# Kernel tuning notes

Hardware: AMD Instinct MI355X
Metric: run time of the kernel (lower is better)

The kernel has to match this reference:

```python
import jax, jax.numpy as jnp
import numpy as np

WINDOW_SIZE = 11
SIGMA = 1.5
C1 = 0.01 ** 2
C2 = 0.03 ** 2


def _gaussian_1d(window_size, sigma):
    x = np.arange(window_size, dtype=np.float32)
    g = np.exp(-((x - window_size // 2) ** 2) / (2.0 * sigma ** 2))
    g = g / g.sum()
    return jnp.asarray(g, dtype=jnp.float32)


def _blur(x, g1d):
    # Separable depthwise Gaussian blur, SAME padding.
    # x: [B, C, H, W]; mathematically identical to conv with outer(g, g).
    c = x.shape[1]
    pad = WINDOW_SIZE // 2
    kh = jnp.broadcast_to(g1d.reshape(1, 1, WINDOW_SIZE, 1), (c, 1, WINDOW_SIZE, 1))
    kw = jnp.broadcast_to(g1d.reshape(1, 1, 1, WINDOW_SIZE), (c, 1, 1, WINDOW_SIZE))
    dn = ('NCHW', 'OIHW', 'NCHW')
    x = jax.lax.conv_general_dilated(x, kh, (1, 1), [(pad, pad), (0, 0)],
                                     dimension_numbers=dn, feature_group_count=c)
    x = jax.lax.conv_general_dilated(x, kw, (1, 1), [(0, 0), (pad, pad)],
                                     dimension_numbers=dn, feature_group_count=c)
    return x


def setup_inputs() -> dict:
    key = jax.random.key(0)
    k1, k2 = jax.random.split(key)
    shape = (32, 1, 512, 512)
    img1 = jax.random.uniform(k1, shape, dtype=jnp.float32)
    img2 = jax.random.uniform(k2, shape, dtype=jnp.float32)
    return {"img1": img1, "img2": img2}


def reference(img1, img2):
    g1d = _gaussian_1d(WINDOW_SIZE, SIGMA)
    mu1 = _blur(img1, g1d)
    mu2 = _blur(img2, g1d)
    mu1_sq = mu1 * mu1
    mu2_sq = mu2 * mu2
    mu1_mu2 = mu1 * mu2
    sigma1_sq = _blur(img1 * img1, g1d) - mu1_sq
    sigma2_sq = _blur(img2 * img2, g1d) - mu2_sq
    sigma12 = _blur(img1 * img2, g1d) - mu1_mu2
    ssim_map = ((2.0 * mu1_mu2 + C1) * (2.0 * sigma12 + C2)) / (
        (mu1_sq + mu2_sq + C1) * (sigma1_sq + sigma2_sq + C2))
    return ssim_map.mean()  # size_average=True
```

## Files before the change

### kernel.cpp

```cpp
#include <hip/hip_runtime.h>

#define HH 512
#define WW 512
#define BATCH 32
#define BH 16
#define NB (HH / BH)
#define TPB 256
#define NBLOCKS (NB * BATCH)
#define CBASE 0xAAAAAAAAu


__global__ __launch_bounds__(TPB) void ssim_main(
    const float* __restrict__ img1,
    const float* __restrict__ img2,
    unsigned* __restrict__ counter,
    float* __restrict__ partial,
    float* __restrict__ out)
{
  constexpr float G[11] = {
      0.00102838f, 0.00759876f, 0.03600077f, 0.10936070f, 0.21300553f,
      0.26601171f,
      0.21300553f, 0.10936070f, 0.03600077f, 0.00759876f, 0.00102838f};
  constexpr float C1 = 1.0e-4f;
  constexpr float C2 = 9.0e-4f;

  const int tid  = threadIdx.x;
  const int L    = tid & 63;
  const int rr   = tid >> 6;
  const int band = blockIdx.x;
  const int bat  = blockIdx.y;
  const int r0   = band * BH;
  const float* p1 = img1 + (size_t)bat * (HH * WW);
  const float* p2 = img2 + (size_t)bat * (HH * WW);
  const int c0 = tid * 2;

  __shared__ __align__(16) float4 pbuf4[4 * 5 * 128];
  float* sp = (float*)pbuf4;

  const int wu4  = tid >> 1;
  const int wOff = ((wu4 ^ ((wu4 >> 3) & 1)) << 2) + ((tid & 1) << 1);

  const int uLo = (2 * L - 2 < 0) ? 0 : 2 * L - 2;
  const int u0  = (2 * L - 1 < 0) ? 0 : 2 * L - 1;
  const int u1  = 2 * L;
  const int u2  = 2 * L + 1;
  const int u3  = (2 * L + 2 > 127) ? 127 : 2 * L + 2;
  const int uHi = (2 * L + 3 > 127) ? 127 : 2 * L + 3;
  const int sLo = ((uLo ^ ((uLo >> 3) & 1)) << 2) + 3;
  const int s0  = (u0 ^ ((u0 >> 3) & 1)) << 2;
  const int s1  = (u1 ^ ((u1 >> 3) & 1)) << 2;
  const int s2  = (u2 ^ ((u2 >> 3) & 1)) << 2;
  const int s3  = (u3 ^ ((u3 >> 3) & 1)) << 2;
  const int sHi = (uHi ^ ((uHi >> 3) & 1)) << 2;

  auto hblur = [&](int a, float (&h)[8]) {
    const int base = (rr * 5 + a) << 9;
    float x[18];
    x[0] = sp[base + sLo];
    const float4 X0 = *(const float4*)(sp + base + s0);
    const float4 X1 = *(const float4*)(sp + base + s1);
    const float4 X2 = *(const float4*)(sp + base + s2);
    const float4 X3 = *(const float4*)(sp + base + s3);
    x[17] = sp[base + sHi];
    x[1] = X0.x;  x[2] = X0.y;  x[3] = X0.z;  x[4] = X0.w;
    x[5] = X1.x;  x[6] = X1.y;  x[7] = X1.z;  x[8] = X1.w;
    x[9] = X2.x;  x[10] = X2.y; x[11] = X2.z; x[12] = X2.w;
    x[13] = X3.x; x[14] = X3.y; x[15] = X3.z; x[16] = X3.w;
    if (L == 0)  { x[0] = x[1] = x[2] = x[3] = x[4] = 0.f; }
    if (L == 63) { x[13] = x[14] = x[15] = x[16] = x[17] = 0.f; }
#pragma unroll
    for (int j = 0; j < 8; ++j) {
      float hv = 0.f;
#pragma unroll
      for (int k = 0; k < 11; ++k) hv = fmaf(G[k], x[j + k], hv);
      h[j] = hv;
    }
  };

  float2 w1[14], w2[14];
#pragma unroll
  for (int j = 0; j < 14; ++j) {
    const int r = r0 - 5 + j;
    float2 a = make_float2(0.f, 0.f), b = a;
    if (r >= 0 && r < HH) {
      a = *(const float2*)(p1 + r * WW + c0);
      b = *(const float2*)(p2 + r * WW + c0);
    }
    w1[j] = a; w2[j] = b;
  }

  float ssum = 0.f;

#pragma unroll 1
  for (int q = 0; q < BH; q += 4) {
    float2 t1[4], t2[4];
#pragma unroll
    for (int j = 0; j < 4; ++j) { t1[j] = make_float2(0.f, 0.f); t2[j] = t1[j]; }
    if (q + 4 < BH) {
#pragma unroll
      for (int j = 0; j < 4; ++j) {
        const int r = r0 + q + 9 + j;
        if (r < HH) {
          t1[j] = *(const float2*)(p1 + r * WW + c0);
          t2[j] = *(const float2*)(p2 + r * WW + c0);
        }
      }
    }

    float acc[4][5][2];
#pragma unroll
    for (int r = 0; r < 4; ++r)
#pragma unroll
      for (int a = 0; a < 5; ++a) { acc[r][a][0] = 0.f; acc[r][a][1] = 0.f; }

#pragma unroll
    for (int e = 0; e < 14; ++e) {
      const float2 xa = w1[e];
      const float2 ya = w2[e];
      const float xv[2] = {xa.x, xa.y};
      const float yv[2] = {ya.x, ya.y};
#pragma unroll
      for (int i = 0; i < 2; ++i) {
        const float x  = xv[i], y = yv[i];
        const float xx = x * x, yy = y * y, xy = x * y;
#pragma unroll
        for (int r = 0; r < 4; ++r) {
          if (e >= r && e <= r + 10) {
            const float g = G[e - r];
            acc[r][0][i] = fmaf(g, x,  acc[r][0][i]);
            acc[r][1][i] = fmaf(g, y,  acc[r][1][i]);
            acc[r][2][i] = fmaf(g, xx, acc[r][2][i]);
            acc[r][3][i] = fmaf(g, yy, acc[r][3][i]);
            acc[r][4][i] = fmaf(g, xy, acc[r][4][i]);
          }
        }
      }
    }

#pragma unroll
    for (int r = 0; r < 4; ++r)
#pragma unroll
      for (int a = 0; a < 5; ++a)
        *(float2*)(sp + ((r * 5 + a) << 9) + wOff) =
            make_float2(acc[r][a][0], acc[r][a][1]);

#pragma unroll
    for (int j = 0; j < 10; ++j) { w1[j] = w1[j + 4]; w2[j] = w2[j + 4]; }
#pragma unroll
    for (int j = 0; j < 4; ++j) { w1[10 + j] = t1[j]; w2[10 + j] = t2[j]; }

    __syncthreads();

    float mu12[8], den1[8], vs[8];
    {
      float ha[8], hb[8];
      hblur(0, ha);
      hblur(1, hb);
#pragma unroll
      for (int j = 0; j < 8; ++j) {
        mu12[j] = ha[j] * hb[j];
        den1[j] = fmaf(ha[j], ha[j], fmaf(hb[j], hb[j], C1));
        vs[j]   = C2 - (den1[j] - C1);
      }
      hblur(2, ha);
      hblur(3, hb);
#pragma unroll
      for (int j = 0; j < 8; ++j) vs[j] += ha[j] + hb[j];
      hblur(4, ha);
#pragma unroll
      for (int j = 0; j < 8; ++j) {
        const float sg12 = ha[j] - mu12[j];
        const float num = fmaf(2.f, mu12[j], C1) * fmaf(2.f, sg12, C2);
        const float den = den1[j] * vs[j];
        float rn = __builtin_amdgcn_rcpf(den);
        rn = rn * fmaf(-den, rn, 2.0f);
        ssum = fmaf(num, rn, ssum);
      }
    }

    __syncthreads();
  }

#pragma unroll
  for (int off = 32; off > 0; off >>= 1) ssum += __shfl_xor(ssum, off, 64);
  float*  wred = sp;
  double* dred = (double*)(sp + 8);
  int*    flag = (int*)(sp + 16);
  if (L == 0) wred[rr] = ssum;
  __syncthreads();
  if (tid == 0) {
    const float bsum = wred[0] + wred[1] + wred[2] + wred[3];
    atomicExch(&partial[bat * NB + band], bsum);
    __threadfence();
    const unsigned old = atomicAdd(counter, 1u);
    flag[0] = (old == CBASE + (unsigned)NBLOCKS - 1u) ? 1 : 0;
  }
  __syncthreads();
  if (flag[0]) {
    double s = 0.0;
    for (int i = tid; i < NBLOCKS; i += TPB)
      s += (double)atomicAdd(&partial[i], 0.0f);
#pragma unroll
    for (int off = 32; off > 0; off >>= 1) s += __shfl_xor(s, off, 64);
    if (L == 0) dred[rr] = s;
    __syncthreads();
    if (tid == 0)
      out[0] = (float)((dred[0] + dred[1] + dred[2] + dred[3]) /
                       (double)((size_t)BATCH * HH * WW));
  }
}

extern "C" void kernel_launch(void* const* d_in, const int* in_sizes, int n_in,
                              void* d_out, int out_size, void* d_ws, size_t ws_size,
                              hipStream_t stream) {
  const float* img1 = (const float*)d_in[0];
  const float* img2 = (const float*)d_in[1];
  float* out = (float*)d_out;
  unsigned* counter = (unsigned*)d_ws;
  float* partial = (float*)((char*)d_ws + 16);
  dim3 grid(NB, BATCH);
  ssim_main<<<grid, TPB, 0, stream>>>(img1, img2, counter, partial, out);
}
```

Baseline: 133.6 us.

## Use four-row bands with 512 threads, one column per thread, no inner loop

Shrinks each block's band from 16 rows to 4 and doubles threads per block to 512, so each thread handles one column for the vertical pass and four outputs in the horizontal pass. The row-sliding loop with register prefetch goes away, and the grid grows fourfold so more blocks are in flight to hide memory latency. In exchange, each 4-row band re-reads 14 input rows, raising global traffic and vertical-blur work about 3.5x, and there are more partials and more atomic counter increments.

```diff
diff --git a/kernel.cpp b/kernel.cpp
--- a/kernel.cpp
+++ b/kernel.cpp
@@ -3,9 +3,9 @@
 #define HH 512
 #define WW 512
 #define BATCH 32
-#define BH 16
+#define BH 4
 #define NB (HH / BH)
-#define TPB 256
+#define TPB 512
 #define NBLOCKS (NB * BATCH)
 #define CBASE 0xAAAAAAAAu
 
@@ -25,51 +25,86 @@
   constexpr float C2 = 9.0e-4f;
 
   const int tid  = threadIdx.x;
-  const int L    = tid & 63;
-  const int rr   = tid >> 6;
   const int band = blockIdx.x;
   const int bat  = blockIdx.y;
   const int r0   = band * BH;
   const float* p1 = img1 + (size_t)bat * (HH * WW);
   const float* p2 = img2 + (size_t)bat * (HH * WW);
-  const int c0 = tid * 2;
 
   __shared__ __align__(16) float4 pbuf4[4 * 5 * 128];
   float* sp = (float*)pbuf4;
 
-  const int wu4  = tid >> 1;
-  const int wOff = ((wu4 ^ ((wu4 >> 3) & 1)) << 2) + ((tid & 1) << 1);
+  {
+    const int col = tid;
+    float acc[4][5];
+#pragma unroll
+    for (int r = 0; r < 4; ++r)
+#pragma unroll
+      for (int a = 0; a < 5; ++a) acc[r][a] = 0.f;
 
-  const int uLo = (2 * L - 2 < 0) ? 0 : 2 * L - 2;
-  const int u0  = (2 * L - 1 < 0) ? 0 : 2 * L - 1;
-  const int u1  = 2 * L;
-  const int u2  = 2 * L + 1;
-  const int u3  = (2 * L + 2 > 127) ? 127 : 2 * L + 2;
-  const int uHi = (2 * L + 3 > 127) ? 127 : 2 * L + 3;
-  const int sLo = ((uLo ^ ((uLo >> 3) & 1)) << 2) + 3;
-  const int s0  = (u0 ^ ((u0 >> 3) & 1)) << 2;
-  const int s1  = (u1 ^ ((u1 >> 3) & 1)) << 2;
-  const int s2  = (u2 ^ ((u2 >> 3) & 1)) << 2;
-  const int s3  = (u3 ^ ((u3 >> 3) & 1)) << 2;
-  const int sHi = (uHi ^ ((uHi >> 3) & 1)) << 2;
+#pragma unroll
+    for (int e = 0; e < 14; ++e) {
+      const int r = r0 - 5 + e;
+      float x = 0.f, y = 0.f;
+      if (r >= 0 && r < HH) {
+        x = p1[r * WW + col];
+        y = p2[r * WW + col];
+      }
+      const float xx = x * x, yy = y * y, xy = x * y;
+#pragma unroll
+      for (int rr = 0; rr < 4; ++rr) {
+        if (e >= rr && e <= rr + 10) {
+          const float g = G[e - rr];
+          acc[rr][0] = fmaf(g, x,  acc[rr][0]);
+          acc[rr][1] = fmaf(g, y,  acc[rr][1]);
+          acc[rr][2] = fmaf(g, xx, acc[rr][2]);
+          acc[rr][3] = fmaf(g, yy, acc[rr][3]);
+          acc[rr][4] = fmaf(g, xy, acc[rr][4]);
+        }
+      }
+    }
 
-  auto hblur = [&](int a, float (&h)[8]) {
+    const int u4   = col >> 2;
+    const int wOff = ((u4 ^ ((u4 >> 3) & 1)) << 2) + (col & 3);
+#pragma unroll
+    for (int r = 0; r < 4; ++r)
+#pragma unroll
+      for (int a = 0; a < 5; ++a)
+        sp[((r * 5 + a) << 9) + wOff] = acc[r][a];
+  }
+
+  __syncthreads();
+
+  const int rr = tid >> 7;
+  const int cg = tid & 127;
+  const int uA = (cg - 2 < 0) ? 0 : cg - 2;
+  const int uB = (cg - 1 < 0) ? 0 : cg - 1;
+  const int uD = (cg + 1 > 127) ? 127 : cg + 1;
+  const int uE = (cg + 2 > 127) ? 127 : cg + 2;
+  const int sA = (uA ^ ((uA >> 3) & 1)) << 2;
+  const int sB = (uB ^ ((uB >> 3) & 1)) << 2;
+  const int sC = (cg ^ ((cg >> 3) & 1)) << 2;
+  const int sD = (uD ^ ((uD >> 3) & 1)) << 2;
+  const int sE = (uE ^ ((uE >> 3) & 1)) << 2;
+
+  auto hblur = [&](int a, float (&h)[4]) {
     const int base = (rr * 5 + a) << 9;
-    float x[18];
-    x[0] = sp[base + sLo];
-    const float4 X0 = *(const float4*)(sp + base + s0);
-    const float4 X1 = *(const float4*)(sp + base + s1);
-    const float4 X2 = *(const float4*)(sp + base + s2);
-    const float4 X3 = *(const float4*)(sp + base + s3);
-    x[17] = sp[base + sHi];
-    x[1] = X0.x;  x[2] = X0.y;  x[3] = X0.z;  x[4] = X0.w;
-    x[5] = X1.x;  x[6] = X1.y;  x[7] = X1.z;  x[8] = X1.w;
-    x[9] = X2.x;  x[10] = X2.y; x[11] = X2.z; x[12] = X2.w;
-    x[13] = X3.x; x[14] = X3.y; x[15] = X3.z; x[16] = X3.w;
-    if (L == 0)  { x[0] = x[1] = x[2] = x[3] = x[4] = 0.f; }
-    if (L == 63) { x[13] = x[14] = x[15] = x[16] = x[17] = 0.f; }
+    const float4 XA = *(const float4*)(sp + base + sA);
+    const float4 XB = *(const float4*)(sp + base + sB);
+    const float4 XC = *(const float4*)(sp + base + sC);
+    const float4 XD = *(const float4*)(sp + base + sD);
+    const float4 XE = *(const float4*)(sp + base + sE);
+    float x[14] = {XA.w,
+                   XB.x, XB.y, XB.z, XB.w,
+                   XC.x, XC.y, XC.z, XC.w,
+                   XD.x, XD.y, XD.z, XD.w,
+                   XE.x};
+    if (cg == 0)   { x[0] = x[1] = x[2] = x[3] = x[4] = 0.f; }
+    if (cg == 1)   { x[0] = 0.f; }
+    if (cg == 126) { x[13] = 0.f; }
+    if (cg == 127) { x[9] = x[10] = x[11] = x[12] = x[13] = 0.f; }
 #pragma unroll
-    for (int j = 0; j < 8; ++j) {
+    for (int j = 0; j < 4; ++j) {
       float hv = 0.f;
 #pragma unroll
       for (int k = 0; k < 11; ++k) hv = fmaf(G[k], x[j + k], hv);
@@ -77,119 +112,47 @@
     }
   };
 
-  float2 w1[14], w2[14];
+  float ssum = 0.f;
+  {
+    float mu12[4], den1[4], vs[4];
+    float ha[4], hb[4];
+    hblur(0, ha);
+    hblur(1, hb);
 #pragma unroll
-  for (int j = 0; j < 14; ++j) {
-    const int r = r0 - 5 + j;
-    float2 a = make_float2(0.f, 0.f), b = a;
-    if (r >= 0 && r < HH) {
-      a = *(const float2*)(p1 + r * WW + c0);
-      b = *(const float2*)(p2 + r * WW + c0);
+    for (int j = 0; j < 4; ++j) {
+      mu12[j] = ha[j] * hb[j];
+      den1[j] = fmaf(ha[j], ha[j], fmaf(hb[j], hb[j], C1));
+      vs[j]   = C2 - (den1[j] - C1);
     }
-    w1[j] = a; w2[j] = b;
-  }
-
-  float ssum = 0.f;
-
-#pragma unroll 1
-  for (int q = 0; q < BH; q += 4) {
-    float2 t1[4], t2[4];
+    hblur(2, ha);
+    hblur(3, hb);
 #pragma unroll
-    for (int j = 0; j < 4; ++j) { t1[j] = make_float2(0.f, 0.f); t2[j] = t1[j]; }
-    if (q + 4 < BH) {
+    for (int j = 0; j < 4; ++j) vs[j] += ha[j] + hb[j];
+    hblur(4, ha);
 #pragma unroll
-      for (int j = 0; j < 4; ++j) {
-        const int r = r0 + q + 9 + j;
-        if (r < HH) {
-          t1[j] = *(const float2*)(p1 + r * WW + c0);
-          t2[j] = *(const float2*)(p2 + r * WW + c0);
-        }
-      }
+    for (int j = 0; j < 4; ++j) {
+      const float sg12 = ha[j] - mu12[j];
+      const float num = fmaf(2.f, mu12[j], C1) * fmaf(2.f, sg12, C2);
+      const float den = den1[j] * vs[j];
+      float rn = __builtin_amdgcn_rcpf(den);
+      rn = rn * fmaf(-den, rn, 2.0f);
+      ssum = fmaf(num, rn, ssum);
     }
-
-    float acc[4][5][2];
-#pragma unroll
-    for (int r = 0; r < 4; ++r)
-#pragma unroll
-      for (int a = 0; a < 5; ++a) { acc[r][a][0] = 0.f; acc[r][a][1] = 0.f; }
-
-#pragma unroll
-    for (int e = 0; e < 14; ++e) {
-      const float2 xa = w1[e];
-      const float2 ya = w2[e];
-      const float xv[2] = {xa.x, xa.y};
-      const float yv[2] = {ya.x, ya.y};
-#pragma unroll
-      for (int i = 0; i < 2; ++i) {
-        const float x  = xv[i], y = yv[i];
-        const float xx = x * x, yy = y * y, xy = x * y;
-#pragma unroll
-        for (int r = 0; r < 4; ++r) {
-          if (e >= r && e <= r + 10) {
-            const float g = G[e - r];
-            acc[r][0][i] = fmaf(g, x,  acc[r][0][i]);
-            acc[r][1][i] = fmaf(g, y,  acc[r][1][i]);
-            acc[r][2][i] = fmaf(g, xx, acc[r][2][i]);
-            acc[r][3][i] = fmaf(g, yy, acc[r][3][i]);
-            acc[r][4][i] = fmaf(g, xy, acc[r][4][i]);
-          }
-        }
-      }
-    }
-
-#pragma unroll
-    for (int r = 0; r < 4; ++r)
-#pragma unroll
-      for (int a = 0; a < 5; ++a)
-        *(float2*)(sp + ((r * 5 + a) << 9) + wOff) =
-            make_float2(acc[r][a][0], acc[r][a][1]);
-
-#pragma unroll
-    for (int j = 0; j < 10; ++j) { w1[j] = w1[j + 4]; w2[j] = w2[j + 4]; }
-#pragma unroll
-    for (int j = 0; j < 4; ++j) { w1[10 + j] = t1[j]; w2[10 + j] = t2[j]; }
-
-    __syncthreads();
-
-    float mu12[8], den1[8], vs[8];
-    {
-      float ha[8], hb[8];
-      hblur(0, ha);
-      hblur(1, hb);
-#pragma unroll
-      for (int j = 0; j < 8; ++j) {
-        mu12[j] = ha[j] * hb[j];
-        den1[j] = fmaf(ha[j], ha[j], fmaf(hb[j], hb[j], C1));
-        vs[j]   = C2 - (den1[j] - C1);
-      }
-      hblur(2, ha);
-      hblur(3, hb);
-#pragma unroll
-      for (int j = 0; j < 8; ++j) vs[j] += ha[j] + hb[j];
-      hblur(4, ha);
-#pragma unroll
-      for (int j = 0; j < 8; ++j) {
-        const float sg12 = ha[j] - mu12[j];
-        const float num = fmaf(2.f, mu12[j], C1) * fmaf(2.f, sg12, C2);
-        const float den = den1[j] * vs[j];
-        float rn = __builtin_amdgcn_rcpf(den);
-        rn = rn * fmaf(-den, rn, 2.0f);
-        ssum = fmaf(num, rn, ssum);
-      }
-    }
-
-    __syncthreads();
   }
 
 #pragma unroll
   for (int off = 32; off > 0; off >>= 1) ssum += __shfl_xor(ssum, off, 64);
+  __syncthreads();
   float*  wred = sp;
-  double* dred = (double*)(sp + 8);
   int*    flag = (int*)(sp + 16);
-  if (L == 0) wred[rr] = ssum;
+  double* dred = (double*)(sp + 24);
+  const int wid = tid >> 6;
+  if ((tid & 63) == 0) wred[wid] = ssum;
   __syncthreads();
   if (tid == 0) {
-    const float bsum = wred[0] + wred[1] + wred[2] + wred[3];
+    float bsum = 0.f;
+#pragma unroll
+    for (int w = 0; w < 8; ++w) bsum += wred[w];
     atomicExch(&partial[bat * NB + band], bsum);
     __threadfence();
     const unsigned old = atomicAdd(counter, 1u);
@@ -202,11 +165,14 @@
       s += (double)atomicAdd(&partial[i], 0.0f);
 #pragma unroll
     for (int off = 32; off > 0; off >>= 1) s += __shfl_xor(s, off, 64);
-    if (L == 0) dred[rr] = s;
+    if ((tid & 63) == 0) dred[wid] = s;
     __syncthreads();
-    if (tid == 0)
-      out[0] = (float)((dred[0] + dred[1] + dred[2] + dred[3]) /
-                       (double)((size_t)BATCH * HH * WW));
+    if (tid == 0) {
+      double t = 0.0;
+#pragma unroll
+      for (int w = 0; w < 8; ++w) t += dred[w];
+      out[0] = (float)(t / (double)((size_t)BATCH * HH * WW));
+    }
   }
 }
 
```

New measurement: 226.3 us. +69.4%, slower.
